# Optimization experiments

Hardware: AMD Instinct MI355X
Metric: run time of the kernel (lower is better)

The kernel has to match this reference:

```python
import jax, jax.numpy as jnp
import numpy as np


def _xavier(key, shape):
    fan_out, fan_in = shape[0], shape[1]
    lim = np.sqrt(6.0 / (fan_in + fan_out)).astype(np.float32)
    return jax.random.uniform(key, shape, jnp.float32, -lim, lim)


def setup_inputs() -> dict:
    key = jax.random.key(0)
    ks = jax.random.split(key, 28)
    B, D, G, ND = 16384, 32, 6, 8
    V_user, V_item, V_gender, V_age, V_occ, V_genre = 1000000, 100000, 2, 7, 21, 19
    H1, H2 = 128, 64
    deep_in = 6 * D + ND  # 200
    return {
        "user_id": jax.random.randint(ks[0], (B,), 0, V_user),
        "item_id": jax.random.randint(ks[1], (B,), 0, V_item),
        "user_gender": jax.random.randint(ks[2], (B,), 0, V_gender),
        "user_age": jax.random.randint(ks[3], (B,), 0, V_age),
        "user_occupation": jax.random.randint(ks[4], (B,), 0, V_occ),
        "item_genre_ids": jax.random.randint(ks[5], (B, G), 0, V_genre),
        "item_genre_mask": jax.random.randint(ks[6], (B, G), 0, 2).astype(jnp.float32),
        "dense_features": jax.random.normal(ks[7], (B, ND), jnp.float32),
        # first-order (1-dim) embedding tables
        "fo_user": _xavier(ks[8], (V_user, 1)),
        "fo_item": _xavier(ks[9], (V_item, 1)),
        "fo_gender": _xavier(ks[10], (V_gender, 1)),
        "fo_age": _xavier(ks[11], (V_age, 1)),
        "fo_occ": _xavier(ks[12], (V_occ, 1)),
        "fo_genre": _xavier(ks[13], (V_genre, 1)),
        # second-order / deep embedding tables
        "emb_user": _xavier(ks[14], (V_user, D)),
        "emb_item": _xavier(ks[15], (V_item, D)),
        "emb_gender": _xavier(ks[16], (V_gender, D)),
        "emb_age": _xavier(ks[17], (V_age, D)),
        "emb_occ": _xavier(ks[18], (V_occ, D)),
        "emb_genre": _xavier(ks[19], (V_genre, D)),
        # dense linear + deep MLP
        "dense_W": _xavier(ks[20], (1, ND)),
        "dense_b": jnp.zeros((1,), jnp.float32),
        "W1": _xavier(ks[21], (H1, deep_in)),
        "b1": jnp.zeros((H1,), jnp.float32),
        "W2": _xavier(ks[22], (H2, H1)),
        "b2": jnp.zeros((H2,), jnp.float32),
        "Wout": _xavier(ks[23], (1, H2)),
        "bout": jnp.zeros((1,), jnp.float32),
    }


def _pool(table, ids, mask):
    # masked mean-pool over the genre list axis
    e = table[ids]                       # [B, G, d]
    m = mask[..., None]                  # [B, G, 1]
    denom = jnp.clip(m.sum(axis=1), 1.0)  # [B, 1]
    return (e * m).sum(axis=1) / denom   # [B, d]


def reference(user_id, item_id, user_gender, user_age, user_occupation,
              item_genre_ids, item_genre_mask, dense_features,
              fo_user, fo_item, fo_gender, fo_age, fo_occ, fo_genre,
              emb_user, emb_item, emb_gender, emb_age, emb_occ, emb_genre,
              dense_W, dense_b, W1, b1, W2, b2, Wout, bout):
    # FM first order: sum of 1-dim gathers + pooled genre + dense linear -> [B,1]
    first = (fo_user[user_id] + fo_item[item_id] + fo_gender[user_gender]
             + fo_age[user_age] + fo_occ[user_occupation]
             + _pool(fo_genre, item_genre_ids, item_genre_mask)
             + dense_features @ dense_W.T + dense_b)
    # FM second order: stack field embeddings [B, 6, D]
    x = jnp.stack([emb_user[user_id], emb_item[item_id], emb_gender[user_gender],
                   emb_age[user_age], emb_occ[user_occupation],
                   _pool(emb_genre, item_genre_ids, item_genre_mask)], axis=1)
    s = x.sum(axis=1)                                   # [B, D]
    second = 0.5 * (s * s - (x * x).sum(axis=1)).sum(axis=1, keepdims=True)  # [B,1]
    # deep part (dropout is identity in eval mode)
    deep_in = jnp.concatenate([x.reshape(x.shape[0], -1), dense_features], axis=1)
    h = jax.nn.relu(deep_in @ W1.T + b1)
    h = jax.nn.relu(h @ W2.T + b2)
    deep = h @ Wout.T + bout                            # [B,1]
    return (first + second + deep).squeeze(1)           # [B]
```

## Files before the change

### kernel.cpp

```cpp
#include <hip/hip_runtime.h>


#define WAVES_PER_BLOCK 4
#define ROWS_PER_WAVE 8
#define ROWS_PER_BLOCK (WAVES_PER_BLOCK * ROWS_PER_WAVE)

__global__ void pack_weights(const float* __restrict__ W1, const float* __restrict__ W2,
                             float4* __restrict__ W1p, float4* __restrict__ W2p) {
    const int idx = blockIdx.x * blockDim.x + threadIdx.x;
    if (idx < 100 * 64) {
        const int k2 = idx >> 6, l = idx & 63;
        const int j0 = 2 * l, j1 = 2 * l + 1, k0 = 2 * k2, k1 = 2 * k2 + 1;
        W1p[idx] = make_float4(W1[j0 * 200 + k0], W1[j1 * 200 + k0],
                               W1[j0 * 200 + k1], W1[j1 * 200 + k1]);
    }
    if (idx < 32 * 64) {
        const int k4 = idx >> 6, l = idx & 63;
        const float* r = W2 + l * 128 + 4 * k4;
        W2p[idx] = make_float4(r[0], r[1], r[2], r[3]);
    }
}

__global__ __launch_bounds__(256) void deepfm_kernel(
    const int* __restrict__ user_id, const int* __restrict__ item_id,
    const int* __restrict__ gender_, const int* __restrict__ age_,
    const int* __restrict__ occ_, const int* __restrict__ genre_ids,
    const float* __restrict__ genre_mask, const float* __restrict__ dense,
    const float* __restrict__ fo_user, const float* __restrict__ fo_item,
    const float* __restrict__ fo_gender, const float* __restrict__ fo_age,
    const float* __restrict__ fo_occ, const float* __restrict__ fo_genre,
    const float* __restrict__ emb_user, const float* __restrict__ emb_item,
    const float* __restrict__ emb_gender, const float* __restrict__ emb_age,
    const float* __restrict__ emb_occ, const float* __restrict__ emb_genre,
    const float* __restrict__ dense_W, const float* __restrict__ dense_b,
    const float4* __restrict__ W1p, const float* __restrict__ b1,
    const float4* __restrict__ W2p, const float* __restrict__ b2,
    const float* __restrict__ Wout, const float* __restrict__ bout,
    float* __restrict__ out, int B)
{
    __shared__ float lds_di[WAVES_PER_BLOCK][ROWS_PER_WAVE][200];
    __shared__ float lds_rs[WAVES_PER_BLOCK][ROWS_PER_WAVE];

    const int tid = threadIdx.x;
    const int wid = tid >> 6;
    const int lane = tid & 63;
    const int rowBase = blockIdx.x * ROWS_PER_BLOCK + wid * ROWS_PER_WAVE;

    int uid[ROWS_PER_WAVE], iid[ROWS_PER_WAVE], gg[ROWS_PER_WAVE],
        aa[ROWS_PER_WAVE], oo[ROWS_PER_WAVE];
    #pragma unroll
    for (int r = 0; r < ROWS_PER_WAVE; ++r) {
        int row = rowBase + r; if (row >= B) row = B - 1;
        uid[r] = user_id[row]; iid[r] = item_id[row];
        gg[r] = gender_[row];  aa[r] = age_[row];  oo[r] = occ_[row];
    }

    #pragma unroll
    for (int r = 0; r < ROWS_PER_WAVE; ++r) {
        int row = rowBase + r; if (row >= B) row = B - 1;

        int gid[6]; float mk[6]; float msum = 0.f;
        #pragma unroll
        for (int t = 0; t < 6; ++t) {
            gid[t] = genre_ids[row * 6 + t];
            mk[t]  = genre_mask[row * 6 + t];
            msum  += mk[t];
        }
        const float inv_den = 1.0f / fmaxf(msum, 1.0f);

        float pe_sum = 0.f, pe_sq = 0.f;
        {
            float v = (lane < 32) ? emb_user[(size_t)uid[r] * 32 + lane]
                                  : emb_item[(size_t)iid[r] * 32 + (lane - 32)];
            lds_di[wid][r][lane] = v;
            pe_sum += v; pe_sq += v * v;
        }
        {
            float v = (lane < 32) ? emb_gender[gg[r] * 32 + lane]
                                  : emb_age[aa[r] * 32 + (lane - 32)];
            lds_di[wid][r][64 + lane] = v;
            pe_sum += v; pe_sq += v * v;
        }
        {
            float v;
            if (lane < 32) {
                v = emb_occ[oo[r] * 32 + lane];
            } else {
                const int d = lane - 32;
                float s = 0.f;
                #pragma unroll
                for (int t = 0; t < 6; ++t) s += mk[t] * emb_genre[gid[t] * 32 + d];
                v = s * inv_den;
            }
            lds_di[wid][r][128 + lane] = v;
            pe_sum += v; pe_sq += v * v;
        }
        if (lane < 8) lds_di[wid][r][192 + lane] = dense[(size_t)row * 8 + lane];

        float s2 = pe_sum + __shfl_xor(pe_sum, 32);
        float ss = pe_sq  + __shfl_xor(pe_sq, 32);
        float t2 = 0.5f * (s2 * s2 - ss);
        #pragma unroll
        for (int off = 16; off >= 1; off >>= 1) t2 += __shfl_xor(t2, off);

        float fo = fo_user[uid[r]] + fo_item[iid[r]] + fo_gender[gg[r]]
                 + fo_age[aa[r]] + fo_occ[oo[r]];
        float fg = 0.f;
        #pragma unroll
        for (int t = 0; t < 6; ++t) fg += mk[t] * fo_genre[gid[t]];
        fo += fg * inv_den;
        float dd = 0.f;
        #pragma unroll
        for (int j = 0; j < 8; ++j) dd += dense[(size_t)row * 8 + j] * dense_W[j];
        fo += dd + dense_b[0];

        if (lane == 0) lds_rs[wid][r] = fo + t2;
    }
    __syncthreads();

    float acc0[ROWS_PER_WAVE], acc1[ROWS_PER_WAVE];
    #pragma unroll
    for (int r = 0; r < ROWS_PER_WAVE; ++r) { acc0[r] = 0.f; acc1[r] = 0.f; }

    const float4* __restrict__ div_ = reinterpret_cast<const float4*>(&lds_di[wid][0][0]);

    for (int k4 = 0; k4 < 50; ++k4) {
        const float4 w0 = W1p[(2 * k4) * 64 + lane];
        const float4 w1 = W1p[(2 * k4 + 1) * 64 + lane];
        #pragma unroll
        for (int r = 0; r < ROWS_PER_WAVE; ++r) {
            const float4 a = div_[r * 50 + k4];
            acc0[r] += w0.x * a.x + w0.z * a.y + w1.x * a.z + w1.z * a.w;
            acc1[r] += w0.y * a.x + w0.w * a.y + w1.y * a.z + w1.w * a.w;
        }
    }

    __syncthreads();
    float* __restrict__ h1b = &lds_di[wid][0][0];
    {
        const float2 bb = *reinterpret_cast<const float2*>(b1 + 2 * lane);
        #pragma unroll
        for (int r = 0; r < ROWS_PER_WAVE; ++r) {
            reinterpret_cast<float2*>(h1b)[r * 64 + lane] =
                make_float2(fmaxf(acc0[r] + bb.x, 0.f), fmaxf(acc1[r] + bb.y, 0.f));
        }
    }
    __syncthreads();

    float acc2[ROWS_PER_WAVE];
    #pragma unroll
    for (int r = 0; r < ROWS_PER_WAVE; ++r) acc2[r] = 0.f;

    const float4* __restrict__ h1v = reinterpret_cast<const float4*>(h1b);

    for (int k4 = 0; k4 < 32; ++k4) {
        const float4 w = W2p[k4 * 64 + lane];
        #pragma unroll
        for (int r = 0; r < ROWS_PER_WAVE; ++r) {
            const float4 h = h1v[r * 32 + k4];
            acc2[r] += w.x * h.x + w.y * h.y + w.z * h.z + w.w * h.w;
        }
    }

    const float wo = Wout[lane];
    const float bb2 = b2[lane];
    const float bo = bout[0];
    for (int r = 0; r < ROWS_PER_WAVE; ++r) {
        const int row = rowBase + r;
        const float h2 = fmaxf(acc2[r] + bb2, 0.f);
        float v = wo * h2;
        #pragma unroll
        for (int off = 32; off >= 1; off >>= 1) v += __shfl_xor(v, off);
        if (lane == 0 && row < B) out[row] = v + bo + lds_rs[wid][r];
    }
}

extern "C" void kernel_launch(void* const* d_in, const int* in_sizes, int n_in,
                              void* d_out, int out_size, void* d_ws, size_t ws_size,
                              hipStream_t stream) {
    const int B = in_sizes[0];

    float4* W1p = reinterpret_cast<float4*>(d_ws);
    float4* W2p = reinterpret_cast<float4*>((char*)d_ws + 102400);

    pack_weights<<<25, 256, 0, stream>>>(
        (const float*)d_in[22], (const float*)d_in[24], W1p, W2p);

    const int grid = (B + ROWS_PER_BLOCK - 1) / ROWS_PER_BLOCK;
    deepfm_kernel<<<grid, 256, 0, stream>>>(
        (const int*)d_in[0],  (const int*)d_in[1],  (const int*)d_in[2],
        (const int*)d_in[3],  (const int*)d_in[4],  (const int*)d_in[5],
        (const float*)d_in[6],  (const float*)d_in[7],
        (const float*)d_in[8],  (const float*)d_in[9],  (const float*)d_in[10],
        (const float*)d_in[11], (const float*)d_in[12], (const float*)d_in[13],
        (const float*)d_in[14], (const float*)d_in[15], (const float*)d_in[16],
        (const float*)d_in[17], (const float*)d_in[18], (const float*)d_in[19],
        (const float*)d_in[20], (const float*)d_in[21],
        W1p, (const float*)d_in[23],
        W2p, (const float*)d_in[25],
        (const float*)d_in[26], (const float*)d_in[27],
        (float*)d_out, B);
}
```

Baseline: 266.1 us.

## Split MLP output columns across waves with block-shared inputs and packed FMA

The MLP stage is restructured so each wave owns a slice of output neurons (32 of H1, 16 of H2) across all 32 block rows instead of all neurons for its own 8 rows. Weights are repacked per wave slice. Input rows come from block-shared LDS, and the math uses 2-wide vector FMAs (v_pk_fma). This cuts global/L2 weight traffic per wave and raises arithmetic per weight load. The cost is cross-wave LDS partial sums for the final output dot product plus an extra barrier, and LDS reads are no longer wave-private.

```diff
diff --git a/kernel.cpp b/kernel.cpp
--- a/kernel.cpp
+++ b/kernel.cpp
@@ -1,22 +1,27 @@
 #include <hip/hip_runtime.h>
 
+
+typedef float v2f __attribute__((ext_vector_type(2)));
 
 #define WAVES_PER_BLOCK 4
 #define ROWS_PER_WAVE 8
-#define ROWS_PER_BLOCK (WAVES_PER_BLOCK * ROWS_PER_WAVE)
+#define ROWS_PER_BLOCK 32
 
 __global__ void pack_weights(const float* __restrict__ W1, const float* __restrict__ W2,
                              float4* __restrict__ W1p, float4* __restrict__ W2p) {
     const int idx = blockIdx.x * blockDim.x + threadIdx.x;
-    if (idx < 100 * 64) {
-        const int k2 = idx >> 6, l = idx & 63;
-        const int j0 = 2 * l, j1 = 2 * l + 1, k0 = 2 * k2, k1 = 2 * k2 + 1;
-        W1p[idx] = make_float4(W1[j0 * 200 + k0], W1[j1 * 200 + k0],
-                               W1[j0 * 200 + k1], W1[j1 * 200 + k1]);
-    }
-    if (idx < 32 * 64) {
-        const int k4 = idx >> 6, l = idx & 63;
-        const float* r = W2 + l * 128 + 4 * k4;
+    if (idx < 6400) {
+        const int w = idx / 1600, rem = idx % 1600;
+        const int k4 = rem >> 5, jp = rem & 31;
+        const int j = w * 32 + jp;
+        const float* r = W1 + j * 200 + 4 * k4;
+        W1p[idx] = make_float4(r[0], r[1], r[2], r[3]);
+    }
+    if (idx < 2048) {
+        const int w = idx / 512, rem = idx % 512;
+        const int k4 = rem >> 4, jp = rem & 15;
+        const int j = w * 16 + jp;
+        const float* r = W2 + j * 128 + 4 * k4;
         W2p[idx] = make_float4(r[0], r[1], r[2], r[3]);
     }
 }
@@ -38,140 +43,172 @@
     const float* __restrict__ Wout, const float* __restrict__ bout,
     float* __restrict__ out, int B)
 {
-    __shared__ float lds_di[WAVES_PER_BLOCK][ROWS_PER_WAVE][200];
-    __shared__ float lds_rs[WAVES_PER_BLOCK][ROWS_PER_WAVE];
+    __shared__ float lds_di[ROWS_PER_BLOCK][200];
+    __shared__ float lds_rs[ROWS_PER_BLOCK];
+    __shared__ float lds_part[ROWS_PER_BLOCK][WAVES_PER_BLOCK];
 
     const int tid = threadIdx.x;
     const int wid = tid >> 6;
     const int lane = tid & 63;
-    const int rowBase = blockIdx.x * ROWS_PER_BLOCK + wid * ROWS_PER_WAVE;
-
-    int uid[ROWS_PER_WAVE], iid[ROWS_PER_WAVE], gg[ROWS_PER_WAVE],
-        aa[ROWS_PER_WAVE], oo[ROWS_PER_WAVE];
+    const int blockRow0 = blockIdx.x * ROWS_PER_BLOCK;
+
+    {
+        const int rowBase = blockRow0 + wid * ROWS_PER_WAVE;
+        int uid[ROWS_PER_WAVE], iid[ROWS_PER_WAVE], gg[ROWS_PER_WAVE],
+            aa[ROWS_PER_WAVE], oo[ROWS_PER_WAVE];
+        #pragma unroll
+        for (int r = 0; r < ROWS_PER_WAVE; ++r) {
+            int row = rowBase + r; if (row >= B) row = B - 1;
+            uid[r] = user_id[row]; iid[r] = item_id[row];
+            gg[r] = gender_[row];  aa[r] = age_[row];  oo[r] = occ_[row];
+        }
+
+        #pragma unroll
+        for (int r = 0; r < ROWS_PER_WAVE; ++r) {
+            int row = rowBase + r; if (row >= B) row = B - 1;
+            const int ri = wid * ROWS_PER_WAVE + r;
+
+            int gid[6]; float mk[6]; float msum = 0.f;
+            #pragma unroll
+            for (int t = 0; t < 6; ++t) {
+                gid[t] = genre_ids[row * 6 + t];
+                mk[t]  = genre_mask[row * 6 + t];
+                msum  += mk[t];
+            }
+            const float inv_den = 1.0f / fmaxf(msum, 1.0f);
+
+            float pe_sum = 0.f, pe_sq = 0.f;
+            {
+                float v = (lane < 32) ? emb_user[(size_t)uid[r] * 32 + lane]
+                                      : emb_item[(size_t)iid[r] * 32 + (lane - 32)];
+                lds_di[ri][lane] = v;
+                pe_sum += v; pe_sq += v * v;
+            }
+            {
+                float v = (lane < 32) ? emb_gender[gg[r] * 32 + lane]
+                                      : emb_age[aa[r] * 32 + (lane - 32)];
+                lds_di[ri][64 + lane] = v;
+                pe_sum += v; pe_sq += v * v;
+            }
+            {
+                float v;
+                if (lane < 32) {
+                    v = emb_occ[oo[r] * 32 + lane];
+                } else {
+                    const int d = lane - 32;
+                    float s = 0.f;
+                    #pragma unroll
+                    for (int t = 0; t < 6; ++t) s += mk[t] * emb_genre[gid[t] * 32 + d];
+                    v = s * inv_den;
+                }
+                lds_di[ri][128 + lane] = v;
+                pe_sum += v; pe_sq += v * v;
+            }
+            if (lane < 8) lds_di[ri][192 + lane] = dense[(size_t)row * 8 + lane];
+
+            float s2 = pe_sum + __shfl_xor(pe_sum, 32);
+            float ss = pe_sq  + __shfl_xor(pe_sq, 32);
+            float t2 = 0.5f * (s2 * s2 - ss);
+            #pragma unroll
+            for (int off = 16; off >= 1; off >>= 1) t2 += __shfl_xor(t2, off);
+
+            float fo = fo_user[uid[r]] + fo_item[iid[r]] + fo_gender[gg[r]]
+                     + fo_age[aa[r]] + fo_occ[oo[r]];
+            float fg = 0.f;
+            #pragma unroll
+            for (int t = 0; t < 6; ++t) fg += mk[t] * fo_genre[gid[t]];
+            fo += fg * inv_den;
+            float dd = 0.f;
+            #pragma unroll
+            for (int j = 0; j < 8; ++j) dd += dense[(size_t)row * 8 + j] * dense_W[j];
+            fo += dd + dense_b[0];
+
+            if (lane == 0) lds_rs[ri] = fo + t2;
+        }
+    }
+    __syncthreads();
+
+    const int jp1 = lane & 31;
+    const int half = lane >> 5;
+
+    v2f acc[16];
     #pragma unroll
-    for (int r = 0; r < ROWS_PER_WAVE; ++r) {
-        int row = rowBase + r; if (row >= B) row = B - 1;
-        uid[r] = user_id[row]; iid[r] = item_id[row];
-        gg[r] = gender_[row];  aa[r] = age_[row];  oo[r] = occ_[row];
-    }
-
+    for (int rp = 0; rp < 16; ++rp) acc[rp] = (v2f)(0.f);
+
+    {
+        const float4* __restrict__ W1b = W1p + wid * 1600;
+        const float4* __restrict__ dv = reinterpret_cast<const float4*>(&lds_di[0][0]);
+
+        for (int k4 = 0; k4 < 50; ++k4) {
+            const float4 w = W1b[k4 * 32 + jp1];
+            const v2f w01 = { w.x, w.y }, w23 = { w.z, w.w };
+            #pragma unroll
+            for (int rp = 0; rp < 16; ++rp) {
+                const float4 a = dv[(half * 16 + rp) * 50 + k4];
+                const v2f a01 = { a.x, a.y }, a23 = { a.z, a.w };
+                acc[rp] = __builtin_elementwise_fma(w01, a01, acc[rp]);
+                acc[rp] = __builtin_elementwise_fma(w23, a23, acc[rp]);
+            }
+        }
+    }
+    __syncthreads();
+
+    float* __restrict__ h1b = &lds_di[0][0];
+    {
+        const float bb = b1[wid * 32 + jp1];
+        #pragma unroll
+        for (int rp = 0; rp < 16; ++rp) {
+            const float h = fmaxf(acc[rp].x + acc[rp].y + bb, 0.f);
+            h1b[(half * 16 + rp) * 128 + wid * 32 + jp1] = h;
+        }
+    }
+    __syncthreads();
+
+    const int jp2 = lane & 15;
+    const int rg = lane >> 4;
+
+    v2f acc2[8];
     #pragma unroll
-    for (int r = 0; r < ROWS_PER_WAVE; ++r) {
-        int row = rowBase + r; if (row >= B) row = B - 1;
-
-        int gid[6]; float mk[6]; float msum = 0.f;
-        #pragma unroll
-        for (int t = 0; t < 6; ++t) {
-            gid[t] = genre_ids[row * 6 + t];
-            mk[t]  = genre_mask[row * 6 + t];
-            msum  += mk[t];
-        }
-        const float inv_den = 1.0f / fmaxf(msum, 1.0f);
-
-        float pe_sum = 0.f, pe_sq = 0.f;
-        {
-            float v = (lane < 32) ? emb_user[(size_t)uid[r] * 32 + lane]
-                                  : emb_item[(size_t)iid[r] * 32 + (lane - 32)];
-            lds_di[wid][r][lane] = v;
-            pe_sum += v; pe_sq += v * v;
-        }
-        {
-            float v = (lane < 32) ? emb_gender[gg[r] * 32 + lane]
-                                  : emb_age[aa[r] * 32 + (lane - 32)];
-            lds_di[wid][r][64 + lane] = v;
-            pe_sum += v; pe_sq += v * v;
-        }
-        {
-            float v;
-            if (lane < 32) {
-                v = emb_occ[oo[r] * 32 + lane];
-            } else {
-                const int d = lane - 32;
-                float s = 0.f;
-                #pragma unroll
-                for (int t = 0; t < 6; ++t) s += mk[t] * emb_genre[gid[t] * 32 + d];
-                v = s * inv_den;
-            }
-            lds_di[wid][r][128 + lane] = v;
-            pe_sum += v; pe_sq += v * v;
-        }
-        if (lane < 8) lds_di[wid][r][192 + lane] = dense[(size_t)row * 8 + lane];
-
-        float s2 = pe_sum + __shfl_xor(pe_sum, 32);
-        float ss = pe_sq  + __shfl_xor(pe_sq, 32);
-        float t2 = 0.5f * (s2 * s2 - ss);
-        #pragma unroll
-        for (int off = 16; off >= 1; off >>= 1) t2 += __shfl_xor(t2, off);
-
-        float fo = fo_user[uid[r]] + fo_item[iid[r]] + fo_gender[gg[r]]
-                 + fo_age[aa[r]] + fo_occ[oo[r]];
-        float fg = 0.f;
-        #pragma unroll
-        for (int t = 0; t < 6; ++t) fg += mk[t] * fo_genre[gid[t]];
-        fo += fg * inv_den;
-        float dd = 0.f;
-        #pragma unroll
-        for (int j = 0; j < 8; ++j) dd += dense[(size_t)row * 8 + j] * dense_W[j];
-        fo += dd + dense_b[0];
-
-        if (lane == 0) lds_rs[wid][r] = fo + t2;
-    }
-    __syncthreads();
-
-    float acc0[ROWS_PER_WAVE], acc1[ROWS_PER_WAVE];
-    #pragma unroll
-    for (int r = 0; r < ROWS_PER_WAVE; ++r) { acc0[r] = 0.f; acc1[r] = 0.f; }
-
-    const float4* __restrict__ div_ = reinterpret_cast<const float4*>(&lds_di[wid][0][0]);
-
-    for (int k4 = 0; k4 < 50; ++k4) {
-        const float4 w0 = W1p[(2 * k4) * 64 + lane];
-        const float4 w1 = W1p[(2 * k4 + 1) * 64 + lane];
-        #pragma unroll
-        for (int r = 0; r < ROWS_PER_WAVE; ++r) {
-            const float4 a = div_[r * 50 + k4];
-            acc0[r] += w0.x * a.x + w0.z * a.y + w1.x * a.z + w1.z * a.w;
-            acc1[r] += w0.y * a.x + w0.w * a.y + w1.y * a.z + w1.w * a.w;
-        }
-    }
-
-    __syncthreads();
-    float* __restrict__ h1b = &lds_di[wid][0][0];
-    {
-        const float2 bb = *reinterpret_cast<const float2*>(b1 + 2 * lane);
-        #pragma unroll
-        for (int r = 0; r < ROWS_PER_WAVE; ++r) {
-            reinterpret_cast<float2*>(h1b)[r * 64 + lane] =
-                make_float2(fmaxf(acc0[r] + bb.x, 0.f), fmaxf(acc1[r] + bb.y, 0.f));
-        }
-    }
-    __syncthreads();
-
-    float acc2[ROWS_PER_WAVE];
-    #pragma unroll
-    for (int r = 0; r < ROWS_PER_WAVE; ++r) acc2[r] = 0.f;
-
-    const float4* __restrict__ h1v = reinterpret_cast<const float4*>(h1b);
-
-    for (int k4 = 0; k4 < 32; ++k4) {
-        const float4 w = W2p[k4 * 64 + lane];
-        #pragma unroll
-        for (int r = 0; r < ROWS_PER_WAVE; ++r) {
-            const float4 h = h1v[r * 32 + k4];
-            acc2[r] += w.x * h.x + w.y * h.y + w.z * h.z + w.w * h.w;
-        }
-    }
-
-    const float wo = Wout[lane];
-    const float bb2 = b2[lane];
-    const float bo = bout[0];
-    for (int r = 0; r < ROWS_PER_WAVE; ++r) {
-        const int row = rowBase + r;
-        const float h2 = fmaxf(acc2[r] + bb2, 0.f);
-        float v = wo * h2;
-        #pragma unroll
-        for (int off = 32; off >= 1; off >>= 1) v += __shfl_xor(v, off);
-        if (lane == 0 && row < B) out[row] = v + bo + lds_rs[wid][r];
+    for (int ri = 0; ri < 8; ++ri) acc2[ri] = (v2f)(0.f);
+
+    {
+        const float4* __restrict__ W2b = W2p + wid * 512;
+        const float4* __restrict__ h1v = reinterpret_cast<const float4*>(h1b);
+
+        for (int k4 = 0; k4 < 32; ++k4) {
+            const float4 w = W2b[k4 * 16 + jp2];
+            const v2f w01 = { w.x, w.y }, w23 = { w.z, w.w };
+            #pragma unroll
+            for (int ri = 0; ri < 8; ++ri) {
+                const float4 h = h1v[(rg * 8 + ri) * 32 + k4];
+                const v2f h01 = { h.x, h.y }, h23 = { h.z, h.w };
+                acc2[ri] = __builtin_elementwise_fma(w01, h01, acc2[ri]);
+                acc2[ri] = __builtin_elementwise_fma(w23, h23, acc2[ri]);
+            }
+        }
+    }
+
+    {
+        const float bb2 = b2[wid * 16 + jp2];
+        const float wo  = Wout[wid * 16 + jp2];
+        #pragma unroll
+        for (int ri = 0; ri < 8; ++ri) {
+            const float h2 = fmaxf(acc2[ri].x + acc2[ri].y + bb2, 0.f);
+            float v = wo * h2;
+            v += __shfl_xor(v, 1); v += __shfl_xor(v, 2);
+            v += __shfl_xor(v, 4); v += __shfl_xor(v, 8);
+            if (jp2 == 0) lds_part[rg * 8 + ri][wid] = v;
+        }
+    }
+    __syncthreads();
+
+    if (tid < ROWS_PER_BLOCK) {
+        const int row = blockRow0 + tid;
+        if (row < B) {
+            const float deep = lds_part[tid][0] + lds_part[tid][1]
+                             + lds_part[tid][2] + lds_part[tid][3] + bout[0];
+            out[row] = deep + lds_rs[tid];
+        }
     }
 }
 
```

Result: slower. 280.8 us (+5.5%).
